# Performance work log

Hardware: AMD Instinct MI355X
Metric: run time of the kernel (lower is better)

## Reference

```python
import jax, jax.numpy as jnp
import numpy as np

B, S, D = 4, 4096, 1024
H = 16
DH = D // H  # 64, required by the fused kernel


def setup_inputs() -> dict:
    key = jax.random.key(0)
    ks = jax.random.split(key, 5)
    scale = 1.0 / np.sqrt(D)  # xavier-ish init scale for square matrices
    return {
        "x": jax.random.normal(ks[0], (B, S, D), dtype=jnp.float32),
        "Wq": jax.random.normal(ks[1], (D, D), dtype=jnp.float32) * scale,
        "Wk": jax.random.normal(ks[2], (D, D), dtype=jnp.float32) * scale,
        "Wv": jax.random.normal(ks[3], (D, D), dtype=jnp.float32) * scale,
        "Wo": jax.random.normal(ks[4], (D, D), dtype=jnp.float32) * scale,
    }


def reference(x, Wq, Wk, Wv, Wo):
    # Fused QKV projection + linear (non-softmax) attention.
    # Q = x Wq, K = x Wk, V = x Wv, split into H heads of size DH.
    b, s, d = x.shape
    h, dh = H, d // H

    def to_heads(t):
        return t.reshape(b, s, h, dh).transpose(0, 2, 1, 3)  # [B,H,S,dh]

    q = to_heads(jnp.einsum("bsd,de->bse", x, Wq))
    k = to_heads(jnp.einsum("bsd,de->bse", x, Wk))
    v = to_heads(jnp.einsum("bsd,de->bse", x, Wv))

    # Linear attention: O(S * dh^2) per head, never materializes [S,S].
    # out = (1/sqrt(dh)) * Q @ (K^T V)
    scale = 1.0 / jnp.sqrt(jnp.asarray(dh, dtype=x.dtype))
    kv = jnp.einsum("bhsd,bhse->bhde", k, v)          # [B,H,dh,dh]
    out = jnp.einsum("bhsd,bhde->bhse", q, kv) * scale  # [B,H,S,dh]

    # kernel output [B,H,S,dh] -> transpose(1,2) -> view [B,S,D]
    out = out.transpose(0, 2, 1, 3).reshape(b, s, d)
    # out_proj: nn.Linear(D, D, bias=False) -> x @ W.T
    return jnp.einsum("bsd,ed->bse", out, Wo)
```

## Files before the change

### kernel.cpp

```cpp
#include <hip/hip_runtime.h>

typedef unsigned short u16;
typedef unsigned int u32;
typedef u16 u16x8 __attribute__((ext_vector_type(8)));
typedef u16 u16x4 __attribute__((ext_vector_type(4)));
typedef __bf16 bf16x8 __attribute__((ext_vector_type(8)));
typedef float f32x4 __attribute__((ext_vector_type(4)));

__device__ __forceinline__ u16 f2bf(float f) {
    u32 u = __builtin_bit_cast(u32, f);
    u32 r = (u + 0x7fffu + ((u >> 16) & 1u)) >> 16;
    return (u16)r;
}
__device__ __forceinline__ void async16(const u16* g, u16* lds_base) {
    __builtin_amdgcn_global_load_lds(
        (const __attribute__((address_space(1))) void*)g,
        (__attribute__((address_space(3))) void*)lds_base, 16, 0, 0);
}
template <bool SW>
__device__ __forceinline__ f32x4 mf(bf16x8 a, bf16x8 b, f32x4 c) {
    if constexpr (SW) return __builtin_amdgcn_mfma_f32_16x16x32_bf16(b, a, c, 0, 0, 0);
    else              return __builtin_amdgcn_mfma_f32_16x16x32_bf16(a, b, c, 0, 0, 0);
}

#define BAR __builtin_amdgcn_s_barrier()
#define WAITLGK do { asm volatile("s_waitcnt lgkmcnt(0)" ::: "memory"); \
                     __builtin_amdgcn_sched_barrier(0); } while (0)
#define PRIO1 __builtin_amdgcn_s_setprio(1)
#define PRIO0 __builtin_amdgcn_s_setprio(0)
#define VM(n) asm volatile("s_waitcnt vmcnt(" #n ")" ::: "memory")

__global__ __launch_bounds__(256) void prep(
    const float* __restrict__ x, u16* __restrict__ xb, u16* __restrict__ xbT,
    const float* __restrict__ wq, u16* __restrict__ wqb,
    const float* __restrict__ wo, u16* __restrict__ wob,
    const float* __restrict__ wk, const float* __restrict__ wv,
    u16* __restrict__ WkvT) {
    const int bid = blockIdx.x;
    const int t = threadIdx.x;
    if (bid < 16384) {
        __shared__ u16 tile[32][33];
        const int s0 = (bid >> 5) * 32, n0 = (bid & 31) * 32;
        const int tx = t & 31, ty = t >> 5;
#pragma unroll
        for (int r = 0; r < 4; ++r) {
            const int s = s0 + ty + 8 * r;
            const u16 bv = f2bf(x[(size_t)s * 1024 + n0 + tx]);
            xb[(size_t)s * 1024 + n0 + tx] = bv;
            tile[ty + 8 * r][tx] = bv;
        }
        __syncthreads();
        const int b = s0 >> 12;
        const int sl = s0 & 4095;
#pragma unroll
        for (int r = 0; r < 4; ++r) {
            const int n = n0 + ty + 8 * r;
            xbT[((size_t)b * 1024 + n) * 4096 + sl + tx] = tile[tx][ty + 8 * r];
        }
    } else if (bid < 17408) {
        const int b2 = bid - 16384;
        const float* src = b2 < 512 ? wq : wo;
        u16* dst = b2 < 512 ? wqb : wob;
        const long base = b2 < 512 ? b2 : b2 - 512;
        const long idx = (base * 256 + t) * 8;
        float4 a = *(const float4*)(src + idx);
        float4 b = *(const float4*)(src + idx + 4);
        u16x8 o;
        o[0] = f2bf(a.x); o[1] = f2bf(a.y); o[2] = f2bf(a.z); o[3] = f2bf(a.w);
        o[4] = f2bf(b.x); o[5] = f2bf(b.y); o[6] = f2bf(b.z); o[7] = f2bf(b.w);
        *(u16x8*)(dst + idx) = o;
    } else {
        __shared__ float tf[32][33];
        const int b3 = bid - 17408;
        const float* W = (b3 >> 10) == 0 ? wk : wv;
        const int n0 = (b3 & 31) * 32, k0 = ((b3 >> 5) & 31) * 32;
        const int tx = t & 31, ty = t >> 5;
#pragma unroll
        for (int r = 0; r < 4; ++r)
            tf[ty + 8 * r][tx] = W[(size_t)(k0 + ty + 8 * r) * 1024 + n0 + tx];
        __syncthreads();
#pragma unroll
        for (int r = 0; r < 4; ++r) {
            const int n = n0 + ty + 8 * r;
            WkvT[((size_t)(b3 >> 10) * 1024 + n) * 1024 + k0 + tx] =
                f2bf(tf[tx][ty + 8 * r]);
        }
    }
}

__global__ __launch_bounds__(512, 1) void gemmS(
    const u16* __restrict__ A, int lda,
    const u16* __restrict__ Bt, int ldb,
    u16* __restrict__ C, int ldc, int K, int nTN,
    size_t aMask, size_t btStrideB) {
    __shared__ u16 SM[4][2][128 * 64];
    const int tid = threadIdx.x, wid = tid >> 6, lane = tid & 63;
    const int wm = wid >> 2, wn = wid & 3;

    const int nwg = gridDim.x;
    const int orig = blockIdx.x;
    const int id = (orig & 7) * (nwg >> 3) + (orig >> 3);
    const size_t mBase = (size_t)(id / nTN) * 128;
    const size_t nBase = (size_t)(id % nTN) * 128;
    const size_t mA = mBase & aMask;
    Bt += (mBase >> 10) * btStrideB;

    const int srow = lane >> 3;
    const int scol = ((lane & 7) ^ (srow & 7)) * 8;

    auto stageS = [&](int buf, int kt) {
#pragma unroll
        for (int c = 0; c < 2; ++c) {
            const u16* g = c ? Bt : A;
            const int ld = c ? ldb : lda;
            const size_t rb = c ? nBase : mA;
            u16* lds = SM[buf][c];
#pragma unroll
            for (int j = 0; j < 2; ++j) {
                const int rowL = wid * 16 + j * 8;
                async16(g + (rb + rowL + srow) * (size_t)ld + (size_t)kt * 64 + scol,
                        lds + rowL * 64);
            }
        }
    };

    const int frow = lane & 15;
    const int xs0 = ((lane >> 4) ^ (frow & 7)) * 8;
    const int xs1 = ((4 + (lane >> 4)) ^ (frow & 7)) * 8;
    f32x4 acc[4][2] = {};

    const int nk = K >> 6;
    stageS(0, 0); stageS(1, 1); stageS(2, 2);
    VM(8);
    BAR;

    for (int kt = 0; kt < nk; ++kt) {
        const int cur = kt & 3;
        if (kt + 3 < nk) stageS((kt + 3) & 3, kt + 3);
        bf16x8 aF[4][2], bF[2][2];
#pragma unroll
        for (int mi = 0; mi < 4; ++mi) {
            const int rA = (wm * 64 + mi * 16 + frow) * 64;
            aF[mi][0] = *(const bf16x8*)&SM[cur][0][rA + xs0];
            aF[mi][1] = *(const bf16x8*)&SM[cur][0][rA + xs1];
        }
#pragma unroll
        for (int ni = 0; ni < 2; ++ni) {
            const int rB = (wn * 32 + ni * 16 + frow) * 64;
            bF[ni][0] = *(const bf16x8*)&SM[cur][1][rB + xs0];
            bF[ni][1] = *(const bf16x8*)&SM[cur][1][rB + xs1];
        }
        WAITLGK;
        PRIO1;
#pragma unroll
        for (int mi = 0; mi < 4; ++mi)
#pragma unroll
            for (int ni = 0; ni < 2; ++ni)
#pragma unroll
                for (int s = 0; s < 2; ++s)
                    acc[mi][ni] = mf<true>(aF[mi][s], bF[ni][s], acc[mi][ni]);
        PRIO0;
        if (kt + 3 < nk)      { VM(8); }
        else if (kt + 2 < nk) { VM(4); }
        else if (kt + 1 < nk) { VM(0); }
        BAR;
    }

    const int rb4 = (lane >> 4) * 4, cx = lane & 15;
#pragma unroll
    for (int mi = 0; mi < 4; ++mi) {
        const size_t row = mBase + wm * 64 + mi * 16 + cx;
#pragma unroll
        for (int ni = 0; ni < 2; ++ni) {
            const size_t col = nBase + wn * 32 + ni * 16 + rb4;
            u16x4 v;
            v[0] = f2bf(acc[mi][ni][0]); v[1] = f2bf(acc[mi][ni][1]);
            v[2] = f2bf(acc[mi][ni][2]); v[3] = f2bf(acc[mi][ni][3]);
            *(u16x4*)&C[row * (size_t)ldc + col] = v;
        }
    }
}

#define As SM[0]
#define Bs SM[1]

#define LDA(buf, mh) do { _Pragma("unroll") for (int mi = 0; mi < 4; ++mi) { \
    const int rA = (wm * 128 + (mh) * 64 + mi * 16 + frow) * 64; \
    aF[mi][0] = *(const bf16x8*)&As[buf][rA + xs0]; \
    aF[mi][1] = *(const bf16x8*)&As[buf][rA + xs1]; } } while (0)

#define LDB(buf, nh) do { _Pragma("unroll") for (int ni = 0; ni < 2; ++ni) { \
    const int rB = (wn * 64 + (nh) * 32 + ni * 16 + frow) * 64; \
    bF[(nh) * 2 + ni][0] = *(const bf16x8*)&Bs[buf][rB + xs0]; \
    bF[(nh) * 2 + ni][1] = *(const bf16x8*)&Bs[buf][rB + xs1]; } } while (0)

#define MFQ(mh, nh) do { _Pragma("unroll") for (int mi = 0; mi < 4; ++mi) \
  _Pragma("unroll") for (int ni = 0; ni < 2; ++ni) \
  _Pragma("unroll") for (int s = 0; s < 2; ++s) \
    acc[(mh) * 4 + mi][(nh) * 2 + ni] = mf<true>( \
        aF[mi][s], bF[(nh) * 2 + ni][s], acc[(mh) * 4 + mi][(nh) * 2 + ni]); } while (0)

#define TILE4(buf, S2, S3, S4, W1, W2, WV) \
  LDA(buf, 0); LDB(buf, 0); BAR; WAITLGK; PRIO1; MFQ(0, 0); PRIO0; W1; BAR; \
  LDB(buf, 1); S2; BAR; WAITLGK; PRIO1; MFQ(0, 1); PRIO0; W2; BAR; \
  LDA(buf, 1); S3; BAR; WAITLGK; PRIO1; MFQ(1, 1); PRIO0; BAR; \
  S4; BAR; WAITLGK; PRIO1; MFQ(1, 0); PRIO0; WV; BAR;

__global__ __launch_bounds__(512, 2) void gemm8p(
    const u16* __restrict__ A, int lda,
    const u16* __restrict__ Bt, int ldb,
    float* __restrict__ Cq, int ldc, int K, int nTN,
    size_t btStrideB) {
    __shared__ u16 SM[2][2][256 * 64];
    const int tid = threadIdx.x;
    const int wid = tid >> 6, lane = tid & 63;
    const int wm = wid >> 2, wn = wid & 3;

    const int nwg = gridDim.x;
    const int orig = blockIdx.x;
    const int id = (orig & 7) * (nwg >> 3) + (orig >> 3);
    const size_t mBase = (size_t)(id / nTN) * 256;
    const size_t nBase = (size_t)(id % nTN) * 256;

    Bt += (mBase >> 12) * btStrideB;

    const int srow = lane >> 3;
    const int scol = (((lane & 7) ^ (srow & 7)) * 8);

    auto stageH = [&](int buf, int isB, int h, int kt) {
        const u16* g = isB ? Bt : A;
        const int ld = isB ? ldb : lda;
        const size_t rb = isB ? nBase : mBase;
        u16* lds = isB ? Bs[buf] : As[buf];
#pragma unroll
        for (int j = 0; j < 2; ++j) {
            const int rowL = isB ? ((wid >> 1) * 64 + h * 32 + (wid & 1) * 16 + j * 8)
                                 : ((wid >> 2) * 128 + h * 64 + (wid & 3) * 16 + j * 8);
            async16(g + (rb + rowL + srow) * (size_t)ld + (size_t)kt * 64 + scol,
                    lds + rowL * 64);
        }
    };

    const int frow = lane & 15;
    const int xs0 = (((lane >> 4)) ^ (frow & 7)) * 8;
    const int xs1 = ((4 + (lane >> 4)) ^ (frow & 7)) * 8;

    f32x4 acc[8][4] = {};
    bf16x8 aF[4][2], bF[4][2];

#pragma unroll
    for (int h = 0; h < 2; ++h) { stageH(0, 0, h, 0); stageH(0, 1, h, 0); }
#pragma unroll
    for (int h = 0; h < 2; ++h) { stageH(1, 0, h, 1); stageH(1, 1, h, 1); }
    VM(8);
    BAR;

    const int np = K >> 7;
    for (int p = 0; p < np - 1; ++p) {
        const int k2 = 2 * p + 2, k3 = 2 * p + 3;
        TILE4(0,
              { stageH(0, 0, 0, k2); stageH(0, 1, 0, k2); },
              stageH(0, 1, 1, k2),
              stageH(0, 0, 1, k2),
              VM(10), VM(12), VM(12));
        TILE4(1,
              { stageH(1, 0, 0, k3); stageH(1, 1, 0, k3); },
              stageH(1, 1, 1, k3),
              stageH(1, 0, 1, k3),
              VM(10), VM(12), VM(12));
    }
    TILE4(0, , , , , , VM(0));
    TILE4(1, , , , , , );

    const int rb4 = (lane >> 4) * 4;
    const int cx = lane & 15;
#pragma unroll
    for (int m = 0; m < 8; ++m) {
        const size_t row = mBase + wm * 128 + m * 16 + cx;
#pragma unroll
        for (int n = 0; n < 4; ++n) {
            const size_t col = nBase + wn * 64 + n * 16 + rb4;
            *(float4*)&Cq[row * (size_t)ldc + col] = *(float4*)&acc[m][n];
        }
    }
}

__global__ __launch_bounds__(256, 2) void kvw2(
    const u16* __restrict__ M1v, const u16* __restrict__ WvT,
    const u16* __restrict__ Wob, u16* __restrict__ W2t) {
    __shared__ u16 Ks[64 * 64];
    __shared__ u16 Vs[64 * 64];
    __shared__ u16 kvs[64 * 64];
    __shared__ u16 Aw[256 * 64];
    const int h = blockIdx.x, b = blockIdx.y;
    const int tid = threadIdx.x, w = tid >> 6, lane = tid & 63;
    const int srow = lane >> 3;
    const int scol = ((lane & 7) ^ srow) * 8;
    const int frow = lane & 15;
    const int xs0 = ((lane >> 4) ^ (frow & 7)) * 8;
    const int xs1 = ((4 + (lane >> 4)) ^ (frow & 7)) * 8;
    const u16* Ap = M1v + (size_t)b * 1048576 + (size_t)h * 64 * 1024;
    const u16* Bp = WvT + (size_t)h * 64 * 1024;
    f32x4 acc[4] = {};
    for (int kk = 0; kk < 16; ++kk) {
        __syncthreads();
#pragma unroll
        for (int j = 0; j < 2; ++j) {
            const int row = w * 16 + j * 8;
            async16(Ap + (size_t)(row + srow) * 1024 + kk * 64 + scol, &Ks[row * 64]);
            async16(Bp + (size_t)(row + srow) * 1024 + kk * 64 + scol, &Vs[row * 64]);
        }
        VM(0);
        __syncthreads();
        bf16x8 a0 = *(const bf16x8*)&Ks[(w * 16 + frow) * 64 + xs0];
        bf16x8 a1 = *(const bf16x8*)&Ks[(w * 16 + frow) * 64 + xs1];
#pragma unroll
        for (int n = 0; n < 4; ++n) {
            bf16x8 b0 = *(const bf16x8*)&Vs[(n * 16 + frow) * 64 + xs0];
            bf16x8 b1 = *(const bf16x8*)&Vs[(n * 16 + frow) * 64 + xs1];
            acc[n] = mf<false>(a0, b0, acc[n]);
            acc[n] = mf<false>(a1, b1, acc[n]);
        }
    }
    {
        const int rb4 = (lane >> 4) * 4, cx = lane & 15;
#pragma unroll
        for (int n = 0; n < 4; ++n) {
            const int col = n * 16 + cx;
            const int unit = col >> 3;
#pragma unroll
            for (int r = 0; r < 4; ++r) {
                const int row = w * 16 + rb4 + r;
                const int byteoff = row * 128 + (((unit ^ (row & 7)) << 4) | ((col & 7) << 1));
                *(u16*)((char*)kvs + byteoff) = f2bf(acc[n][r] * 0.125f);
            }
        }
    }
    __syncthreads();
    u16* outB = W2t + (size_t)b * 1048576;
    for (int eT = 0; eT < 4; ++eT) {
#pragma unroll
        for (int j = 0; j < 8; ++j) {
            const int row = w * 64 + j * 8;
            async16(Wob + (size_t)(eT * 256 + row + srow) * 1024 + h * 64 + scol,
                    &Aw[row * 64]);
        }
        VM(0);
        __syncthreads();
        f32x4 a2[4][4] = {};
#pragma unroll
        for (int m = 0; m < 4; ++m) {
            bf16x8 a0 = *(const bf16x8*)&Aw[(w * 64 + m * 16 + frow) * 64 + xs0];
            bf16x8 a1 = *(const bf16x8*)&Aw[(w * 64 + m * 16 + frow) * 64 + xs1];
#pragma unroll
            for (int n = 0; n < 4; ++n) {
                bf16x8 b0 = *(const bf16x8*)&kvs[(n * 16 + frow) * 64 + xs0];
                bf16x8 b1 = *(const bf16x8*)&kvs[(n * 16 + frow) * 64 + xs1];
                a2[m][n] = mf<false>(a0, b0, a2[m][n]);
                a2[m][n] = mf<false>(a1, b1, a2[m][n]);
            }
        }
        const int rb4 = (lane >> 4) * 4, cx = lane & 15;
#pragma unroll
        for (int m = 0; m < 4; ++m)
#pragma unroll
            for (int n = 0; n < 4; ++n)
#pragma unroll
                for (int r = 0; r < 4; ++r)
                    outB[(size_t)(eT * 256 + w * 64 + m * 16 + rb4 + r) * 1024 +
                         h * 64 + n * 16 + cx] = f2bf(a2[m][n][r]);
        __syncthreads();
    }
}

extern "C" void kernel_launch(void* const* d_in, const int* in_sizes, int n_in,
                              void* d_out, int out_size, void* d_ws, size_t ws_size,
                              hipStream_t stream) {
    const float* x  = (const float*)d_in[0];
    const float* Wq = (const float*)d_in[1];
    const float* Wk = (const float*)d_in[2];
    const float* Wv = (const float*)d_in[3];
    const float* Wo = (const float*)d_in[4];
    float* out = (float*)d_out;
    char* ws = (char*)d_ws;

    u16* xb   = (u16*)(ws);
    u16* xbT  = (u16*)(ws + 33554432);
    u16* G    = (u16*)(ws + 67108864);
    u16* M1v  = (u16*)(ws + 75497472);
    u16* WkvT = (u16*)(ws + 83886080);
    u16* Wqb  = (u16*)(ws + 88080384);
    u16* Wob  = (u16*)(ws + 90177536);
    u16* W2t  = (u16*)(ws + 92798976);
    u16* W3T  = (u16*)(ws + 101187584);
    u16* WkT  = WkvT;
    u16* WvT  = WkvT + 1048576;

    prep<<<19456, 256, 0, stream>>>(x, xb, xbT, Wq, Wqb, Wo, Wob, Wk, Wv, WkvT);

    gemmS<<<256, 512, 0, stream>>>(xbT, 4096, xbT, 4096, G, 1024, 4096, 8,
                                   ~0ULL, 4194304ULL);
    gemmS<<<256, 512, 0, stream>>>(WkT, 1024, G, 1024, M1v, 1024, 1024, 8,
                                   1023ULL, 1048576ULL);
    kvw2<<<dim3(16, 4), 256, 0, stream>>>(M1v, WvT, Wob, W2t);
    gemmS<<<256, 512, 0, stream>>>(W2t, 1024, Wqb, 1024, W3T, 1024, 1024, 8,
                                   ~0ULL, 0ULL);
    gemm8p<<<256, 512, 0, stream>>>(xb, 1024, W3T, 1024, out, 1024, 1024, 4, 1048576ULL);
}
```

Measured before the change: 157.7 us.

## Restructure final GEMM pipeline with separate lo/hi fragments and next-tile A prefetch

The final 256x256 GEMM replaces the TILE4 schedule with a new F_TILE schedule. It keeps separate aLo/aHi/bLo/bHi register fragments, reorders the MFMA quadrants so fragments are reused across consecutive quadrants, and prefetches the next buffer's A-low fragment during the last quadrant. The goal is to hide LDS read latency and cut redundant fragment reloads, at the cost of more VGPRs, which could hurt occupancy at 2 waves/SIMD. The async staging order and vmcnt waits also change, which adds some risk of ordering mistakes.

```diff
diff --git a/kernel.cpp b/kernel.cpp
--- a/kernel.cpp
+++ b/kernel.cpp
@@ -181,32 +181,42 @@
     }
 }
 
-#define As SM[0]
-#define Bs SM[1]
-
-#define LDA(buf, mh) do { _Pragma("unroll") for (int mi = 0; mi < 4; ++mi) { \
-    const int rA = (wm * 128 + (mh) * 64 + mi * 16 + frow) * 64; \
-    aF[mi][0] = *(const bf16x8*)&As[buf][rA + xs0]; \
-    aF[mi][1] = *(const bf16x8*)&As[buf][rA + xs1]; } } while (0)
-
-#define LDB(buf, nh) do { _Pragma("unroll") for (int ni = 0; ni < 2; ++ni) { \
-    const int rB = (wn * 64 + (nh) * 32 + ni * 16 + frow) * 64; \
-    bF[(nh) * 2 + ni][0] = *(const bf16x8*)&Bs[buf][rB + xs0]; \
-    bF[(nh) * 2 + ni][1] = *(const bf16x8*)&Bs[buf][rB + xs1]; } } while (0)
-
-#define MFQ(mh, nh) do { _Pragma("unroll") for (int mi = 0; mi < 4; ++mi) \
+#define F_LDALO(buf) do { _Pragma("unroll") for (int mi = 0; mi < 4; ++mi) { \
+    const int rA = (wm * 128 + mi * 16 + frow) * 64; \
+    aLo[mi][0] = *(const bf16x8*)&SM[buf][0][rA + xs0]; \
+    aLo[mi][1] = *(const bf16x8*)&SM[buf][0][rA + xs1]; } } while (0)
+#define F_LDAHI(buf) do { _Pragma("unroll") for (int mi = 0; mi < 4; ++mi) { \
+    const int rA = (wm * 128 + 64 + mi * 16 + frow) * 64; \
+    aHi[mi][0] = *(const bf16x8*)&SM[buf][0][rA + xs0]; \
+    aHi[mi][1] = *(const bf16x8*)&SM[buf][0][rA + xs1]; } } while (0)
+#define F_LDBLO(buf) do { _Pragma("unroll") for (int ni = 0; ni < 2; ++ni) { \
+    const int rB = (wn * 64 + ni * 16 + frow) * 64; \
+    bLo[ni][0] = *(const bf16x8*)&SM[buf][1][rB + xs0]; \
+    bLo[ni][1] = *(const bf16x8*)&SM[buf][1][rB + xs1]; } } while (0)
+#define F_LDBHI(buf) do { _Pragma("unroll") for (int ni = 0; ni < 2; ++ni) { \
+    const int rB = (wn * 64 + 32 + ni * 16 + frow) * 64; \
+    bHi[ni][0] = *(const bf16x8*)&SM[buf][1][rB + xs0]; \
+    bHi[ni][1] = *(const bf16x8*)&SM[buf][1][rB + xs1]; } } while (0)
+#define F_MFQ(AM, BM, mo, no) do { _Pragma("unroll") for (int mi = 0; mi < 4; ++mi) \
   _Pragma("unroll") for (int ni = 0; ni < 2; ++ni) \
   _Pragma("unroll") for (int s = 0; s < 2; ++s) \
-    acc[(mh) * 4 + mi][(nh) * 2 + ni] = mf<true>( \
-        aF[mi][s], bF[(nh) * 2 + ni][s], acc[(mh) * 4 + mi][(nh) * 2 + ni]); } while (0)
-
-#define TILE4(buf, S2, S3, S4, W1, W2, WV) \
-  LDA(buf, 0); LDB(buf, 0); BAR; WAITLGK; PRIO1; MFQ(0, 0); PRIO0; W1; BAR; \
-  LDB(buf, 1); S2; BAR; WAITLGK; PRIO1; MFQ(0, 1); PRIO0; W2; BAR; \
-  LDA(buf, 1); S3; BAR; WAITLGK; PRIO1; MFQ(1, 1); PRIO0; BAR; \
-  S4; BAR; WAITLGK; PRIO1; MFQ(1, 0); PRIO0; WV; BAR;
-
-__global__ __launch_bounds__(512, 2) void gemm8p(
+    acc[(mo) + mi][(no) + ni] = mf<true>(AM[mi][s], BM[ni][s], acc[(mo) + mi][(no) + ni]); } while (0)
+
+#define F_TILE(c, stg, look, kt2) do { \
+  F_LDBLO(c); if (stg) stageR(c, 0, 0, kt2); \
+  BAR; WAITLGK; PRIO1; F_MFQ(aLo, bLo, 0, 0); PRIO0; BAR; \
+  F_LDBHI(c); \
+  BAR; WAITLGK; PRIO1; F_MFQ(aLo, bHi, 0, 2); PRIO0; \
+  if (stg) { VM(8); } else { VM(0); } BAR; \
+  F_LDAHI(c); if (stg) stageR(c, 1, 0, kt2); \
+  BAR; WAITLGK; PRIO1; F_MFQ(aHi, bHi, 4, 2); PRIO0; BAR; \
+  if (look) F_LDALO((c) ^ 1); \
+  if (stg) { stageR(c, 1, 1, kt2); stageR(c, 0, 1, kt2); } \
+  BAR; WAITLGK; PRIO1; F_MFQ(aHi, bLo, 4, 0); PRIO0; \
+  if (stg) { VM(8); } else { VM(0); } BAR; \
+} while (0)
+
+__global__ __launch_bounds__(512, 2) void gemm8f(
     const u16* __restrict__ A, int lda,
     const u16* __restrict__ Bt, int ldb,
     float* __restrict__ Cq, int ldc, int K, int nTN,
@@ -225,13 +235,13 @@
     Bt += (mBase >> 12) * btStrideB;
 
     const int srow = lane >> 3;
-    const int scol = (((lane & 7) ^ (srow & 7)) * 8);
-
-    auto stageH = [&](int buf, int isB, int h, int kt) {
+    const int scol = ((lane & 7) ^ (srow & 7)) * 8;
+
+    auto stageR = [&](int buf, int isB, int h, int kt) {
         const u16* g = isB ? Bt : A;
         const int ld = isB ? ldb : lda;
         const size_t rb = isB ? nBase : mBase;
-        u16* lds = isB ? Bs[buf] : As[buf];
+        u16* lds = SM[buf][isB];
 #pragma unroll
         for (int j = 0; j < 2; ++j) {
             const int rowL = isB ? ((wid >> 1) * 64 + h * 32 + (wid & 1) * 16 + j * 8)
@@ -242,35 +252,26 @@
     };
 
     const int frow = lane & 15;
-    const int xs0 = (((lane >> 4)) ^ (frow & 7)) * 8;
+    const int xs0 = ((lane >> 4) ^ (frow & 7)) * 8;
     const int xs1 = ((4 + (lane >> 4)) ^ (frow & 7)) * 8;
 
     f32x4 acc[8][4] = {};
-    bf16x8 aF[4][2], bF[4][2];
-
-#pragma unroll
-    for (int h = 0; h < 2; ++h) { stageH(0, 0, h, 0); stageH(0, 1, h, 0); }
-#pragma unroll
-    for (int h = 0; h < 2; ++h) { stageH(1, 0, h, 1); stageH(1, 1, h, 1); }
+    bf16x8 aLo[4][2], aHi[4][2], bLo[2][2], bHi[2][2];
+
+#pragma unroll
+    for (int b = 0; b < 2; ++b) {
+        stageR(b, 0, 0, b); stageR(b, 0, 1, b);
+        stageR(b, 1, 0, b); stageR(b, 1, 1, b);
+    }
     VM(8);
     BAR;
-
-    const int np = K >> 7;
-    for (int p = 0; p < np - 1; ++p) {
-        const int k2 = 2 * p + 2, k3 = 2 * p + 3;
-        TILE4(0,
-              { stageH(0, 0, 0, k2); stageH(0, 1, 0, k2); },
-              stageH(0, 1, 1, k2),
-              stageH(0, 0, 1, k2),
-              VM(10), VM(12), VM(12));
-        TILE4(1,
-              { stageH(1, 0, 0, k3); stageH(1, 1, 0, k3); },
-              stageH(1, 1, 1, k3),
-              stageH(1, 0, 1, k3),
-              VM(10), VM(12), VM(12));
-    }
-    TILE4(0, , , , , , VM(0));
-    TILE4(1, , , , , , );
+    F_LDALO(0);
+
+    const int nt = K >> 6;
+    for (int t = 0; t < nt; t += 2) {
+        F_TILE(0, (t + 2 < nt), true, t + 2);
+        F_TILE(1, (t + 3 < nt), (t + 2 < nt), t + 3);
+    }
 
     const int rb4 = (lane >> 4) * 4;
     const int cx = lane & 15;
@@ -405,5 +406,5 @@
     kvw2<<<dim3(16, 4), 256, 0, stream>>>(M1v, WvT, Wob, W2t);
     gemmS<<<256, 512, 0, stream>>>(W2t, 1024, Wqb, 1024, W3T, 1024, 1024, 8,
                                    ~0ULL, 0ULL);
-    gemm8p<<<256, 512, 0, stream>>>(xb, 1024, W3T, 1024, out, 1024, 1024, 4, 1048576ULL);
-}
+    gemm8f<<<256, 512, 0, stream>>>(xb, 1024, W3T, 1024, out, 1024, 1024, 4, 1048576ULL);
+}
```

Result: slower. 169.9 us (+7.7%).

## Split-K the Gram GEMM into two halves with fp32 partials and reduce

Applied to the files above, without the earlier changes.

The first GEMM (x^T x Gram per batch, K=4096) is split along K into two halves, launched as 512 workgroups instead of 256. Each half writes fp32 partials, and a new addcvt kernel sums them and converts to bf16. The goal is better CU occupancy on a GPU with more CUs than the original 256 tiles. The cost is extra fp32 partial traffic (two 16MB buffers) and an additional kernel launch.

```diff
diff --git a/kernel.cpp b/kernel.cpp
--- a/kernel.cpp
+++ b/kernel.cpp
@@ -88,22 +88,35 @@
     }
 }
 
+__device__ __forceinline__ void stc4(u16* p, f32x4 v) {
+    u16x4 o; o[0] = f2bf(v[0]); o[1] = f2bf(v[1]); o[2] = f2bf(v[2]); o[3] = f2bf(v[3]);
+    *(u16x4*)p = o;
+}
+__device__ __forceinline__ void stc4(float* p, f32x4 v) { *(f32x4*)p = v; }
+
+template <typename OutT>
 __global__ __launch_bounds__(512, 1) void gemmS(
     const u16* __restrict__ A, int lda,
     const u16* __restrict__ Bt, int ldb,
-    u16* __restrict__ C, int ldc, int K, int nTN,
-    size_t aMask, size_t btStrideB) {
+    OutT* __restrict__ C, int ldc, int K, int nTN,
+    size_t aMask, size_t btStrideB, int kSplit, size_t cStrideH) {
     __shared__ u16 SM[4][2][128 * 64];
     const int tid = threadIdx.x, wid = tid >> 6, lane = tid & 63;
     const int wm = wid >> 2, wn = wid & 3;
 
     const int nwg = gridDim.x;
     const int orig = blockIdx.x;
-    const int id = (orig & 7) * (nwg >> 3) + (orig >> 3);
+    int id = (orig & 7) * (nwg >> 3) + (orig >> 3);
+    const int perH = nwg / kSplit;
+    const int half = id / perH;
+    id -= half * perH;
     const size_t mBase = (size_t)(id / nTN) * 128;
     const size_t nBase = (size_t)(id % nTN) * 128;
     const size_t mA = mBase & aMask;
-    Bt += (mBase >> 10) * btStrideB;
+    const size_t kOff = (size_t)half * K;
+    A += kOff;
+    Bt += (mBase >> 10) * btStrideB + kOff;
+    C += (size_t)half * cStrideH;
 
     const int srow = lane >> 3;
     const int scol = ((lane & 7) ^ (srow & 7)) * 8;
@@ -173,12 +186,21 @@
 #pragma unroll
         for (int ni = 0; ni < 2; ++ni) {
             const size_t col = nBase + wn * 32 + ni * 16 + rb4;
-            u16x4 v;
-            v[0] = f2bf(acc[mi][ni][0]); v[1] = f2bf(acc[mi][ni][1]);
-            v[2] = f2bf(acc[mi][ni][2]); v[3] = f2bf(acc[mi][ni][3]);
-            *(u16x4*)&C[row * (size_t)ldc + col] = v;
-        }
-    }
+            stc4(&C[row * (size_t)ldc + col], acc[mi][ni]);
+        }
+    }
+}
+
+__global__ __launch_bounds__(256) void addcvt(
+    const float* __restrict__ P0, const float* __restrict__ P1,
+    u16* __restrict__ G) {
+    const long i = ((long)blockIdx.x * 256 + threadIdx.x) * 4;
+    f32x4 a = *(const f32x4*)(P0 + i);
+    f32x4 b = *(const f32x4*)(P1 + i);
+    f32x4 s = a + b;
+    u16x4 o;
+    o[0] = f2bf(s[0]); o[1] = f2bf(s[1]); o[2] = f2bf(s[2]); o[3] = f2bf(s[3]);
+    *(u16x4*)(G + i) = o;
 }
 
 #define As SM[0]
@@ -384,26 +406,29 @@
     float* out = (float*)d_out;
     char* ws = (char*)d_ws;
 
-    u16* xb   = (u16*)(ws);
-    u16* xbT  = (u16*)(ws + 33554432);
-    u16* G    = (u16*)(ws + 67108864);
-    u16* M1v  = (u16*)(ws + 75497472);
-    u16* WkvT = (u16*)(ws + 83886080);
-    u16* Wqb  = (u16*)(ws + 88080384);
-    u16* Wob  = (u16*)(ws + 90177536);
-    u16* W2t  = (u16*)(ws + 92798976);
-    u16* W3T  = (u16*)(ws + 101187584);
-    u16* WkT  = WkvT;
-    u16* WvT  = WkvT + 1048576;
+    u16*   xb   = (u16*)(ws);
+    u16*   xbT  = (u16*)(ws + 33554432);
+    u16*   G    = (u16*)(ws + 67108864);
+    u16*   M1v  = (u16*)(ws + 75497472);
+    u16*   WkvT = (u16*)(ws + 83886080);
+    u16*   Wqb  = (u16*)(ws + 88080384);
+    u16*   Wob  = (u16*)(ws + 90177536);
+    u16*   W2t  = (u16*)(ws + 92798976);
+    u16*   W3T  = (u16*)(ws + 101187584);
+    float* Gp   = (float*)(ws + 109576192);
+    u16*   WkT  = WkvT;
+    u16*   WvT  = WkvT + 1048576;
 
     prep<<<19456, 256, 0, stream>>>(x, xb, xbT, Wq, Wqb, Wo, Wob, Wk, Wv, WkvT);
 
-    gemmS<<<256, 512, 0, stream>>>(xbT, 4096, xbT, 4096, G, 1024, 4096, 8,
-                                   ~0ULL, 4194304ULL);
-    gemmS<<<256, 512, 0, stream>>>(WkT, 1024, G, 1024, M1v, 1024, 1024, 8,
-                                   1023ULL, 1048576ULL);
+    gemmS<float><<<512, 512, 0, stream>>>(xbT, 4096, xbT, 4096, Gp, 1024, 2048, 8,
+                                          ~0ULL, 4194304ULL, 2, 4194304ULL);
+    addcvt<<<4096, 256, 0, stream>>>(Gp, Gp + 4194304, G);
+
+    gemmS<u16><<<256, 512, 0, stream>>>(WkT, 1024, G, 1024, M1v, 1024, 1024, 8,
+                                        1023ULL, 1048576ULL, 1, 0);
     kvw2<<<dim3(16, 4), 256, 0, stream>>>(M1v, WvT, Wob, W2t);
-    gemmS<<<256, 512, 0, stream>>>(W2t, 1024, Wqb, 1024, W3T, 1024, 1024, 8,
-                                   ~0ULL, 0ULL);
+    gemmS<u16><<<256, 512, 0, stream>>>(W2t, 1024, Wqb, 1024, W3T, 1024, 1024, 8,
+                                        ~0ULL, 0ULL, 1, 0);
     gemm8p<<<256, 512, 0, stream>>>(xb, 1024, W3T, 1024, out, 1024, 1024, 4, 1048576ULL);
 }
```

Measured after the change: 171.6 us. 1.09x slower.
